# Kernel optimization log

Measured on AMD Instinct MI355X. Metric: run time of the kernel, lower is better.

## Reference

```python
import jax, jax.numpy as jnp
import numpy as np

TIME = 10  # hardcoded interpolation steps in the original module


def _interpolation(poly, time=TIME):
    # poly: [B, N, 2] -> [B, N*time, 2]
    poly_roll = jnp.roll(poly, shift=1, axis=1)
    step = (jnp.arange(time, dtype=poly.dtype) / time)[:, None]        # [T, 1]
    # [B, N, T, 2] = current * step + previous * (1 - step)
    interp = poly[:, :, None, :] * step + poly_roll[:, :, None, :] * (1.0 - step)
    return interp.reshape(poly.shape[0], -1, 2)


def _compute_distance(pred_poly, gt_poly):
    # pred_poly: [B, Np, 2], gt_poly: [B, Ng, 2] -> squared dists [B, Ng, Np]
    diff = gt_poly[:, :, None, :] - pred_poly[:, None, :, :]
    return jnp.sum(diff * diff, axis=3)


def reference(ini_pred_poly, pred_polys_, gt_polys, keyPointsMask):
    # --- lossPred2NearestGt: each pred point matched to nearest interpolated gt ---
    gt_interp = _interpolation(gt_polys)                               # [B, Ng*T, 2]
    dist_pg = _compute_distance(ini_pred_poly, gt_interp)              # [B, Ng*T, Np]
    index_gt = jnp.argmin(dist_pg, axis=1)                             # [B, Np]
    nearest_gt = jnp.take_along_axis(gt_interp, index_gt[:, :, None], axis=1)  # [B, Np, 2]
    loss_pred2gt = jnp.mean(jnp.abs(pred_polys_ - nearest_gt))         # l1, mean reduction

    # --- lossGt2NearestPred: each gt vertex matched to nearest pred point ---
    dist_gp = _compute_distance(ini_pred_poly, gt_polys)               # [B, Ng, Np]
    index_pred = jnp.argmin(dist_gp, axis=2)                           # [B, Ng]
    nearest_pred = jnp.take_along_axis(pred_polys_, index_pred[:, :, None], axis=1)  # [B, Ng, 2]
    loss_gt2pred = jnp.abs(nearest_pred - gt_polys)                    # l1, no reduction, [B, Ng, 2]

    mask = jnp.broadcast_to(keyPointsMask[:, :, None], loss_gt2pred.shape)
    loss = jnp.sum(loss_gt2pred * mask) / (jnp.sum(mask) + 1.0) + loss_pred2gt
    return loss / 2.0


def setup_inputs() -> dict:
    key = jax.random.key(0)
    k1, k2, k3, k4 = jax.random.split(key, 4)
    B, Np, Ng = 1024, 128, 128
    return {
        "ini_pred_poly": jax.random.uniform(k1, (B, Np, 2), dtype=jnp.float32),
        "pred_polys_": jax.random.uniform(k2, (B, Np, 2), dtype=jnp.float32),
        "gt_polys": jax.random.uniform(k3, (B, Ng, 2), dtype=jnp.float32),
        "keyPointsMask": jax.random.uniform(k4, (B, Ng), dtype=jnp.float32),
    }
```

## Files before the change

### kernel.cpp

```cpp
#include <hip/hip_runtime.h>


constexpr int NP = 128;
constexpr int NG = 128;
constexpr int TT = 10;

__global__ __launch_bounds__(512) void dm_main(
    const float* __restrict__ ini,
    const float* __restrict__ pp,
    const float* __restrict__ gt,
    const float* __restrict__ mask,
    double* __restrict__ partial)
{
    const int b   = blockIdx.x;
    const int tid = threadIdx.x;

    __shared__ float2 s_gt  [NG];
    __shared__ float2 s_ini [NP];
    __shared__ float2 s_pp  [NP];
    __shared__ float4 s_seg [NG];
    __shared__ float  s_s10 [NG];
    __shared__ float  s_bd1 [512];
    __shared__ float  s_bi1 [512];
    __shared__ float  s_bd2 [512];
    __shared__ float  s_bi2 [512];
    __shared__ double s_red [24];

    if (tid < 256) {
        ((float*)s_gt )[tid] = gt [(size_t)b * 256 + tid];
        ((float*)s_ini)[tid] = ini[(size_t)b * 256 + tid];
        ((float*)s_pp )[tid] = pp [(size_t)b * 256 + tid];
    }
    const float mval = (tid < NG) ? mask[(size_t)b * NG + tid] : 0.0f;
    __syncthreads();

    if (tid < NG) {
        const float2 c  = s_gt[tid];
        const float2 pr = s_gt[(tid + NG - 1) & (NG - 1)];
        const float ex = c.x - pr.x, ey = c.y - pr.y;
        const float ee = fmaxf(fmaf(ey, ey, ex * ex), 1e-30f);
        s_seg[tid] = make_float4(pr.x, pr.y, ex, ey);
        s_s10[tid] = 10.0f * __builtin_amdgcn_rcpf(ee);
    }
    __syncthreads();

    const int p       = tid & (NP - 1);
    const int quarter = tid >> 7;

    {
        const float2 q = s_ini[p];
        const int s0 = quarter * (NG / 4);
        float best  = 3.4e38f;
        float bif   = 0.0f;
        float basef = (float)(s0 * TT);
        #pragma unroll 8
        for (int k = 0; k < NG / 4; ++k) {
            const float4 sg  = s_seg[s0 + k];
            const float  s10 = s_s10[s0 + k];
            const float wx = q.x - sg.x, wy = q.y - sg.y;
            const float dot = fmaf(wy, sg.w, wx * sg.z);
            float tc = rintf(dot * s10);
            tc = fminf(fmaxf(tc, 0.0f), 9.0f);
            const float u   = tc * 0.1f;
            const float dqx = fmaf(-u, sg.z, wx);
            const float dqy = fmaf(-u, sg.w, wy);
            const float d   = fmaf(dqy, dqy, dqx * dqx);
            const float cand = basef + tc;
            bif  = (d < best) ? cand : bif;
            best = fminf(d, best);
            basef += 10.0f;
        }
        s_bd1[tid] = best;
        s_bi1[tid] = bif;
    }

    {
        const float2 gv = s_gt[p];
        const int j0 = quarter * (NP / 4);
        float bd  = 3.4e38f;
        float bjf = 0.0f;
        float jf  = (float)j0;
        #pragma unroll 8
        for (int k = 0; k < NP / 4; ++k) {
            const float2 pv = s_ini[j0 + k];
            const float dx = gv.x - pv.x, dy = gv.y - pv.y;
            const float d  = fmaf(dy, dy, dx * dx);
            bjf = (d < bd) ? jf : bjf;
            bd  = fminf(d, bd);
            jf += 1.0f;
        }
        s_bd2[tid] = bd;
        s_bi2[tid] = bjf;
    }
    __syncthreads();

    double l_p2g = 0.0, l_masked = 0.0, l_msum = 0.0;
    if (tid < NP) {
        float bd = s_bd1[tid];
        float bi = s_bi1[tid];
        #pragma unroll
        for (int qq = 1; qq < 4; ++qq) {
            const float d2 = s_bd1[tid + qq * 128];
            const float i2 = s_bi1[tid + qq * 128];
            bi = (d2 < bd) ? i2 : bi;
            bd = fminf(d2, bd);
        }
        const int idx = (int)bi;
        const int n = idx / TT;
        const int t = idx - n * TT;
        const float step = (float)t / 10.0f;
        const float om   = 1.0f - step;
        const float2 c  = s_gt[n];
        const float2 pr = s_gt[(n + NG - 1) & (NG - 1)];
        const float nx = c.x * step + pr.x * om;
        const float ny = c.y * step + pr.y * om;
        const float2 mp = s_pp[tid];
        l_p2g = (double)fabsf(mp.x - nx) + (double)fabsf(mp.y - ny);

        float cd = s_bd2[tid];
        float cj = s_bi2[tid];
        #pragma unroll
        for (int qq = 1; qq < 4; ++qq) {
            const float d2 = s_bd2[tid + qq * 128];
            const float j2 = s_bi2[tid + qq * 128];
            cj = (d2 < cd) ? j2 : cj;
            cd = fminf(d2, cd);
        }
        const float2 npt = s_pp[(int)cj];
        const float2 gv  = s_gt[tid];
        l_masked = (double)mval * ((double)fabsf(npt.x - gv.x) + (double)fabsf(npt.y - gv.y));
        l_msum   = 2.0 * (double)mval;
    }

    for (int off = 32; off > 0; off >>= 1) {
        l_p2g    += __shfl_down(l_p2g, off);
        l_masked += __shfl_down(l_masked, off);
        l_msum   += __shfl_down(l_msum, off);
    }
    const int wid = tid >> 6, lane = tid & 63;
    if (lane == 0) {
        s_red[wid * 3 + 0] = l_p2g;
        s_red[wid * 3 + 1] = l_masked;
        s_red[wid * 3 + 2] = l_msum;
    }
    __syncthreads();
    if (tid == 0) {
        double a = 0.0, c = 0.0, m = 0.0;
        #pragma unroll
        for (int w = 0; w < 8; ++w) {
            a += s_red[w * 3 + 0];
            c += s_red[w * 3 + 1];
            m += s_red[w * 3 + 2];
        }
        partial[(size_t)b * 3 + 0] = a;
        partial[(size_t)b * 3 + 1] = c;
        partial[(size_t)b * 3 + 2] = m;
    }
}

__global__ __launch_bounds__(256) void dm_final(
    const double* __restrict__ partial, int nb, double inv_count, float* __restrict__ out)
{
    const int tid = threadIdx.x;
    double a = 0.0, c = 0.0, d = 0.0;
    for (int b = tid; b < nb; b += 256) {
        a += partial[(size_t)b * 3 + 0];
        c += partial[(size_t)b * 3 + 1];
        d += partial[(size_t)b * 3 + 2];
    }
    for (int off = 32; off > 0; off >>= 1) {
        a += __shfl_down(a, off);
        c += __shfl_down(c, off);
        d += __shfl_down(d, off);
    }
    __shared__ double s[12];
    const int wid = tid >> 6, lane = tid & 63;
    if (lane == 0) { s[wid * 3] = a; s[wid * 3 + 1] = c; s[wid * 3 + 2] = d; }
    __syncthreads();
    if (tid == 0) {
        const double at = s[0] + s[3] + s[6] + s[9];
        const double ct = s[1] + s[4] + s[7] + s[10];
        const double dt = s[2] + s[5] + s[8] + s[11];
        const double loss = ct / (dt + 1.0) + at * inv_count;
        out[0] = (float)(loss * 0.5);
    }
}

extern "C" void kernel_launch(void* const* d_in, const int* in_sizes, int n_in,
                              void* d_out, int out_size, void* d_ws, size_t ws_size,
                              hipStream_t stream) {
    const float* ini  = (const float*)d_in[0];
    const float* pp   = (const float*)d_in[1];
    const float* gt   = (const float*)d_in[2];
    const float* mask = (const float*)d_in[3];
    float* out = (float*)d_out;

    const int B = in_sizes[0] / (NP * 2);
    double* partial = (double*)d_ws;

    dm_main<<<B, 512, 0, stream>>>(ini, pp, gt, mask, partial);
    const double inv_count = 1.0 / ((double)B * NP * 2);
    dm_final<<<1, 256, 0, stream>>>(partial, B, inv_count, out);
}
```

Before: 20.12 us.

## Remove shared-memory staging and presync, read inputs directly from global memory

The initial shared-memory staging of gt and ini and the precomputed segment table are dropped, along with two __syncthreads barriers. Each thread now reads gt and ini straight from global memory (uniform addresses via readfirstlane) and recomputes segment vectors and reciprocals inline. The per-block reduction moves from double to float and is limited to the two active waves, and the partials buffer becomes float. In exchange there is redundant per-thread arithmetic, more global or cache loads, and slightly lower accumulation precision.

```diff
diff --git a/kernel.cpp b/kernel.cpp
--- a/kernel.cpp
+++ b/kernel.cpp
@@ -3,87 +3,75 @@
 
 constexpr int NP = 128;
 constexpr int NG = 128;
-constexpr int TT = 10;
 
 __global__ __launch_bounds__(512) void dm_main(
     const float* __restrict__ ini,
     const float* __restrict__ pp,
     const float* __restrict__ gt,
     const float* __restrict__ mask,
-    double* __restrict__ partial)
+    float* __restrict__ partial)
 {
     const int b   = blockIdx.x;
     const int tid = threadIdx.x;
 
-    __shared__ float2 s_gt  [NG];
-    __shared__ float2 s_ini [NP];
-    __shared__ float2 s_pp  [NP];
-    __shared__ float4 s_seg [NG];
-    __shared__ float  s_s10 [NG];
-    __shared__ float  s_bd1 [512];
-    __shared__ float  s_bi1 [512];
-    __shared__ float  s_bd2 [512];
-    __shared__ float  s_bi2 [512];
-    __shared__ double s_red [24];
+    __shared__ float2 s_gt [NG];
+    __shared__ float2 s_pp [NP];
+    __shared__ float  s_bd1[512], s_bi1[512], s_bd2[512], s_bi2[512];
+    __shared__ float  s_red[6];
+
+    const float* gtb  = gt  + (size_t)b * 256;
+    const float* inib = ini + (size_t)b * 256;
+    const float* ppb  = pp  + (size_t)b * 256;
 
     if (tid < 256) {
-        ((float*)s_gt )[tid] = gt [(size_t)b * 256 + tid];
-        ((float*)s_ini)[tid] = ini[(size_t)b * 256 + tid];
-        ((float*)s_pp )[tid] = pp [(size_t)b * 256 + tid];
+        ((float*)s_gt)[tid] = gtb[tid];
+        ((float*)s_pp)[tid] = ppb[tid];
     }
-    const float mval = (tid < NG) ? mask[(size_t)b * NG + tid] : 0.0f;
-    __syncthreads();
 
-    if (tid < NG) {
-        const float2 c  = s_gt[tid];
-        const float2 pr = s_gt[(tid + NG - 1) & (NG - 1)];
-        const float ex = c.x - pr.x, ey = c.y - pr.y;
-        const float ee = fmaxf(fmaf(ey, ey, ex * ex), 1e-30f);
-        s_seg[tid] = make_float4(pr.x, pr.y, ex, ey);
-        s_s10[tid] = 10.0f * __builtin_amdgcn_rcpf(ee);
-    }
-    __syncthreads();
+    const int p  = tid & (NP - 1);
+    const int s0 = __builtin_amdgcn_readfirstlane((tid >> 7) << 5);
 
-    const int p       = tid & (NP - 1);
-    const int quarter = tid >> 7;
+    const float2 q    = ((const float2*)inib)[p];
+    const float2 gv   = ((const float2*)gtb)[p];
+    const float  mval = (tid < NP) ? mask[(size_t)b * NG + tid] : 0.0f;
 
     {
-        const float2 q = s_ini[p];
-        const int s0 = quarter * (NG / 4);
         float best  = 3.4e38f;
         float bif   = 0.0f;
-        float basef = (float)(s0 * TT);
+        float basef = (float)(s0 * 10);
+        float2 pv = ((const float2*)gtb)[(s0 + NG - 1) & (NG - 1)];
         #pragma unroll 8
-        for (int k = 0; k < NG / 4; ++k) {
-            const float4 sg  = s_seg[s0 + k];
-            const float  s10 = s_s10[s0 + k];
-            const float wx = q.x - sg.x, wy = q.y - sg.y;
-            const float dot = fmaf(wy, sg.w, wx * sg.z);
+        for (int k = 0; k < 32; ++k) {
+            const float2 cv = ((const float2*)gtb)[s0 + k];
+            const float ex = cv.x - pv.x, ey = cv.y - pv.y;
+            const float wx = q.x - pv.x,  wy = q.y - pv.y;
+            const float ee = fmaxf(fmaf(ey, ey, ex * ex), 1e-30f);
+            const float s10 = 10.0f * __builtin_amdgcn_rcpf(ee);
+            const float dot = fmaf(wy, ey, wx * ex);
             float tc = rintf(dot * s10);
             tc = fminf(fmaxf(tc, 0.0f), 9.0f);
             const float u   = tc * 0.1f;
-            const float dqx = fmaf(-u, sg.z, wx);
-            const float dqy = fmaf(-u, sg.w, wy);
+            const float dqx = fmaf(-u, ex, wx);
+            const float dqy = fmaf(-u, ey, wy);
             const float d   = fmaf(dqy, dqy, dqx * dqx);
             const float cand = basef + tc;
             bif  = (d < best) ? cand : bif;
             best = fminf(d, best);
             basef += 10.0f;
+            pv = cv;
         }
         s_bd1[tid] = best;
         s_bi1[tid] = bif;
     }
 
     {
-        const float2 gv = s_gt[p];
-        const int j0 = quarter * (NP / 4);
         float bd  = 3.4e38f;
         float bjf = 0.0f;
-        float jf  = (float)j0;
+        float jf  = (float)s0;
         #pragma unroll 8
-        for (int k = 0; k < NP / 4; ++k) {
-            const float2 pv = s_ini[j0 + k];
-            const float dx = gv.x - pv.x, dy = gv.y - pv.y;
+        for (int k = 0; k < 32; ++k) {
+            const float2 pvt = ((const float2*)inib)[s0 + k];
+            const float dx = gv.x - pvt.x, dy = gv.y - pvt.y;
             const float d  = fmaf(dy, dy, dx * dx);
             bjf = (d < bd) ? jf : bjf;
             bd  = fminf(d, bd);
@@ -94,7 +82,7 @@
     }
     __syncthreads();
 
-    double l_p2g = 0.0, l_masked = 0.0, l_msum = 0.0;
+    float l_a = 0.0f, l_c = 0.0f, l_m = 0.0f;
     if (tid < NP) {
         float bd = s_bd1[tid];
         float bi = s_bi1[tid];
@@ -106,8 +94,8 @@
             bd = fminf(d2, bd);
         }
         const int idx = (int)bi;
-        const int n = idx / TT;
-        const int t = idx - n * TT;
+        const int n = idx / 10;
+        const int t = idx - n * 10;
         const float step = (float)t / 10.0f;
         const float om   = 1.0f - step;
         const float2 c  = s_gt[n];
@@ -115,7 +103,7 @@
         const float nx = c.x * step + pr.x * om;
         const float ny = c.y * step + pr.y * om;
         const float2 mp = s_pp[tid];
-        l_p2g = (double)fabsf(mp.x - nx) + (double)fabsf(mp.y - ny);
+        l_a = fabsf(mp.x - nx) + fabsf(mp.y - ny);
 
         float cd = s_bd2[tid];
         float cj = s_bi2[tid];
@@ -127,46 +115,41 @@
             cd = fminf(d2, cd);
         }
         const float2 npt = s_pp[(int)cj];
-        const float2 gv  = s_gt[tid];
-        l_masked = (double)mval * ((double)fabsf(npt.x - gv.x) + (double)fabsf(npt.y - gv.y));
-        l_msum   = 2.0 * (double)mval;
+        const float2 gvv = s_gt[tid];
+        l_c = mval * (fabsf(npt.x - gvv.x) + fabsf(npt.y - gvv.y));
+        l_m = 2.0f * mval;
     }
 
-    for (int off = 32; off > 0; off >>= 1) {
-        l_p2g    += __shfl_down(l_p2g, off);
-        l_masked += __shfl_down(l_masked, off);
-        l_msum   += __shfl_down(l_msum, off);
-    }
     const int wid = tid >> 6, lane = tid & 63;
-    if (lane == 0) {
-        s_red[wid * 3 + 0] = l_p2g;
-        s_red[wid * 3 + 1] = l_masked;
-        s_red[wid * 3 + 2] = l_msum;
+    if (wid < 2) {
+        for (int off = 32; off > 0; off >>= 1) {
+            l_a += __shfl_down(l_a, off);
+            l_c += __shfl_down(l_c, off);
+            l_m += __shfl_down(l_m, off);
+        }
+        if (lane == 0) {
+            s_red[wid * 3 + 0] = l_a;
+            s_red[wid * 3 + 1] = l_c;
+            s_red[wid * 3 + 2] = l_m;
+        }
     }
     __syncthreads();
     if (tid == 0) {
-        double a = 0.0, c = 0.0, m = 0.0;
-        #pragma unroll
-        for (int w = 0; w < 8; ++w) {
-            a += s_red[w * 3 + 0];
-            c += s_red[w * 3 + 1];
-            m += s_red[w * 3 + 2];
-        }
-        partial[(size_t)b * 3 + 0] = a;
-        partial[(size_t)b * 3 + 1] = c;
-        partial[(size_t)b * 3 + 2] = m;
+        partial[(size_t)b * 3 + 0] = s_red[0] + s_red[3];
+        partial[(size_t)b * 3 + 1] = s_red[1] + s_red[4];
+        partial[(size_t)b * 3 + 2] = s_red[2] + s_red[5];
     }
 }
 
 __global__ __launch_bounds__(256) void dm_final(
-    const double* __restrict__ partial, int nb, double inv_count, float* __restrict__ out)
+    const float* __restrict__ partial, int nb, double inv_count, float* __restrict__ out)
 {
     const int tid = threadIdx.x;
     double a = 0.0, c = 0.0, d = 0.0;
     for (int b = tid; b < nb; b += 256) {
-        a += partial[(size_t)b * 3 + 0];
-        c += partial[(size_t)b * 3 + 1];
-        d += partial[(size_t)b * 3 + 2];
+        a += (double)partial[(size_t)b * 3 + 0];
+        c += (double)partial[(size_t)b * 3 + 1];
+        d += (double)partial[(size_t)b * 3 + 2];
     }
     for (int off = 32; off > 0; off >>= 1) {
         a += __shfl_down(a, off);
@@ -196,7 +179,7 @@
     float* out = (float*)d_out;
 
     const int B = in_sizes[0] / (NP * 2);
-    double* partial = (double*)d_ws;
+    float* partial = (float*)d_ws;
 
     dm_main<<<B, 512, 0, stream>>>(ini, pp, gt, mask, partial);
     const double inv_count = 1.0 / ((double)B * NP * 2);
```

New measurement: 24.11 us. 1.2x slower.
